# Kernel optimization log

Hardware: AMD Instinct MI355X
Metric: run time of the kernel (lower is better)

Reference implementation:

```python
import math
import jax, jax.numpy as jnp
import numpy as np

EMBED_DIM = 512
NUM_HEADS = 8
HEAD_DIM = EMBED_DIM // NUM_HEADS
NUM_EDGE_TYPES = 10
N = 2048  # nodes
B = 1


def setup_inputs() -> dict:
    key = jax.random.key(0)
    ks = jax.random.split(key, 8)
    s = 1.0 / math.sqrt(EMBED_DIM)
    return {
        "query": jax.random.normal(ks[0], (N, B, EMBED_DIM), jnp.float32),
        "key": jax.random.normal(ks[1], (N, B, EMBED_DIM), jnp.float32),
        "value": jax.random.normal(ks[2], (N, B, EMBED_DIM), jnp.float32),
        "edge_id_mat": jax.random.randint(ks[3], (N, N), 0, NUM_EDGE_TYPES, jnp.int32),
        "in_proj_weight": jax.random.normal(ks[4], (3 * EMBED_DIM, EMBED_DIM), jnp.float32) * s,
        "in_proj_bias": jnp.zeros((3 * EMBED_DIM,), jnp.float32),
        "out_proj_weight": jax.random.normal(ks[5], (EMBED_DIM, EMBED_DIM), jnp.float32) * s,
        "out_proj_bias": jnp.zeros((EMBED_DIM,), jnp.float32),
        "edge_embs_K": jax.random.normal(ks[6], (NUM_EDGE_TYPES, HEAD_DIM), jnp.float32),
    }


def reference(query, key, value, edge_id_mat, in_proj_weight, in_proj_bias,
              out_proj_weight, out_proj_bias, edge_embs_K):
    L, Bsz, E = query.shape
    H, hd = NUM_HEADS, HEAD_DIM
    w_q, w_k, w_v = jnp.split(in_proj_weight, 3, axis=0)
    b_q, b_k, b_v = jnp.split(in_proj_bias, 3)
    q = query @ w_q.T + b_q   # (L, B, E)
    k = key @ w_k.T + b_k
    v = value @ w_v.T + b_v

    def split_heads(x):
        # (L, B, E) -> (B*H, L, hd)  (matches torch view(L, B*H, hd).transpose(0,1))
        return x.reshape(L, Bsz * H, hd).transpose(1, 0, 2)

    q = split_heads(q) / math.sqrt(hd)  # torch scales by sqrt(E=head_dim)
    k = split_heads(k)
    v = split_heads(v)

    attn = jnp.einsum('bnd,bmd->bnm', q, k)  # (B*H, L, L)

    # edge-type score bias: edge_attn[b,i,j] = q[b,i,:] . edge_embs_K[edge_id_mat[i,j], :]
    # computed efficiently as per-type scores then a gather (avoids (L,L,hd) tensor)
    type_scores = jnp.einsum('bnd,td->bnt', q, edge_embs_K)  # (B*H, L, T)
    idx = jnp.broadcast_to(edge_id_mat[None, :, :], attn.shape)
    edge_attn = jnp.take_along_axis(type_scores, idx, axis=2)  # (B*H, L, L)
    attn = jax.nn.softmax(attn + edge_attn, axis=-1)

    out = jnp.einsum('bnm,bmd->bnd', attn, v)           # (B*H, L, hd)
    out = out.transpose(1, 0, 2).reshape(L, Bsz, E)      # (L, B, E)
    out = out @ out_proj_weight.T + out_proj_bias
    return out
```

## Files before the change

kernel.cpp:

```cpp
#include <hip/hip_runtime.h>
#include <hip/hip_bf16.h>

#define NHEAD 8
#define SEQ   2048
#define HD    64
#define EMB   512
#define NTYPE 10
#define JSPLIT 8

#define QKV_NT (3 * EMB / 64)
#define QKV_MT (SEQ / 64)
#define QKV_BLOCKS (QKV_NT * QKV_MT)
#define PACK_BLOCKS (SEQ * SEQ / 4 / 256)

#define QSCALE 0.180336878f

typedef unsigned short u16;
typedef __attribute__((ext_vector_type(8))) short short8;
typedef __attribute__((ext_vector_type(4))) short short4v;
typedef __attribute__((ext_vector_type(4))) float float4v;

union F8 { short8 v; uint4 u4; u16 us[8]; };
union PB { uint2 u2; short4v s4; };

__device__ __forceinline__ float bf2f(u16 u){
  union { unsigned u; float f; } w; w.u = ((unsigned)u) << 16; return w.f;
}
__device__ __forceinline__ u16 f2bf(float f){
  union { float f; unsigned u; } w; w.f = f;
  unsigned u = w.u;
  u += 0x7fffu + ((u >> 16) & 1u);
  return (u16)(u >> 16);
}
__device__ __forceinline__ unsigned cvtpk(float lo, float hi){
  union { __hip_bfloat162 b; unsigned u; } w;
  w.b = __float22bfloat162_rn(float2{lo, hi});
  return w.u;
}
__device__ __forceinline__ uint4 pk8(float4 a, float4 b){
  uint4 p; p.x = cvtpk(a.x, a.y); p.y = cvtpk(a.z, a.w);
           p.z = cvtpk(b.x, b.y); p.w = cvtpk(b.z, b.w);
  return p;
}

__device__ __forceinline__ void pv_mfma(float4v& ao, uint2 pa, uint2 vb){
#if __has_builtin(__builtin_amdgcn_mfma_f32_16x16x16bf16_1k)
  PB a; a.u2 = pa;
  PB b; b.u2 = vb;
  ao = __builtin_amdgcn_mfma_f32_16x16x16bf16_1k(a.s4, b.s4, ao, 0, 0, 0);
#else
  asm volatile("s_nop 1\n\tv_mfma_f32_16x16x16_bf16 %0, %1, %2, %0"
               : "+v"(ao) : "v"(pa), "v"(vb));
#endif
}

__global__ __launch_bounds__(256) void fused_prep_gemm(
    const float* __restrict__ q, const float* __restrict__ k, const float* __restrict__ v,
    const float* __restrict__ ipw, const float* __restrict__ ipb, const int* __restrict__ eid,
    u16* __restrict__ Qs, u16* __restrict__ Kb, u16* __restrict__ Vb,
    unsigned* __restrict__ eidp)
{
  const int b = blockIdx.x;
  const int t = threadIdx.x;

  if (b >= QKV_BLOCKS) {
    const int i = (b - QKV_BLOCKS) * 256 + t;
    int4 vv = ((const int4*)eid)[i];
    eidp[i] = (unsigned)(vv.x & 0xff) | ((unsigned)(vv.y & 0xff) << 8) |
              ((unsigned)(vv.z & 0xff) << 16) | ((unsigned)(vv.w & 0xff) << 24);
    return;
  }

  __shared__ u16 As[64][72];
  __shared__ u16 Bs[64][72];

  const int X = b & 7, jb = b >> 3;
  const int mt = X * 4 + (jb & 3), nt = jb >> 2;
  const int n0 = nt * 64, m0 = mt * 64;
  const int z = n0 >> 9;
  const float* A = (z == 0) ? q : (z == 1) ? k : v;
  const float scale = (z == 0) ? QSCALE : 1.0f;

  const int w = t >> 6, lane = t & 63, lr = lane & 15, lg = lane >> 4;
  const int wm = w >> 1, wn = w & 1;
  const int srow = t >> 2, kb16 = (t & 3) * 16;

  float4v acc[2][2];
#pragma unroll
  for (int mi = 0; mi < 2; mi++)
#pragma unroll
    for (int ni = 0; ni < 2; ni++) acc[mi][ni] = (float4v){0.f, 0.f, 0.f, 0.f};

  const float* pa = A   + (size_t)(m0 + srow) * EMB + kb16;
  const float* pw = ipw + (size_t)(n0 + srow) * EMB + kb16;

  float4 a[4], bb[4];
#pragma unroll
  for (int j = 0; j < 4; j++) { a[j] = *(const float4*)(pa + j * 4); bb[j] = *(const float4*)(pw + j * 4); }

  for (int k0 = 0; k0 < EMB; k0 += 64) {
    *(uint4*)&As[srow][kb16]     = pk8(a[0], a[1]);
    *(uint4*)&As[srow][kb16 + 8] = pk8(a[2], a[3]);
    *(uint4*)&Bs[srow][kb16]     = pk8(bb[0], bb[1]);
    *(uint4*)&Bs[srow][kb16 + 8] = pk8(bb[2], bb[3]);
    __syncthreads();
    if (k0 + 64 < EMB) {
#pragma unroll
      for (int j = 0; j < 4; j++) {
        a[j]  = *(const float4*)(pa + k0 + 64 + j * 4);
        bb[j] = *(const float4*)(pw + k0 + 64 + j * 4);
      }
    }
    F8 af[2][2], bf_[2][2];
#pragma unroll
    for (int kc = 0; kc < 2; kc++) {
#pragma unroll
      for (int mi = 0; mi < 2; mi++)
        af[mi][kc].u4 = *(const uint4*)&As[wm * 32 + mi * 16 + lr][kc * 32 + lg * 8];
#pragma unroll
      for (int ni = 0; ni < 2; ni++)
        bf_[ni][kc].u4 = *(const uint4*)&Bs[wn * 32 + ni * 16 + lr][kc * 32 + lg * 8];
    }
#pragma unroll
    for (int kc = 0; kc < 2; kc++)
#pragma unroll
      for (int mi = 0; mi < 2; mi++)
#pragma unroll
        for (int ni = 0; ni < 2; ni++)
          acc[mi][ni] = __builtin_amdgcn_mfma_f32_16x16x32_bf16(af[mi][kc].v, bf_[ni][kc].v, acc[mi][ni], 0, 0, 0);
    __syncthreads();
  }

  u16* O = (z == 0) ? Qs : ((z == 1) ? Kb : Vb);
#pragma unroll
  for (int mi = 0; mi < 2; mi++) {
#pragma unroll
    for (int ni = 0; ni < 2; ni++) {
      const int n = n0 + wn * 32 + ni * 16 + lr;
      const int e = n & 511, h = e >> 6, d = e & 63;
      const float bias = ipb[n];
      const int mb = m0 + wm * 32 + mi * 16 + lg * 4;
      if (z < 2) {
#pragma unroll
        for (int r = 0; r < 4; r++)
          O[((size_t)h * SEQ + mb + r) * HD + d] = f2bf((acc[mi][ni][r] + bias) * scale);
      } else {
        ushort4 pk;
        pk.x = f2bf(acc[mi][ni][0] + bias); pk.y = f2bf(acc[mi][ni][1] + bias);
        pk.z = f2bf(acc[mi][ni][2] + bias); pk.w = f2bf(acc[mi][ni][3] + bias);
        *(ushort4*)(O + ((size_t)(h * HD + d)) * SEQ + mb) = pk;
      }
    }
  }
}

__global__ __launch_bounds__(256) void attn_kernel(
    const u16* __restrict__ Qs, const u16* __restrict__ Kb, const u16* __restrict__ Vb,
    const unsigned* __restrict__ eid32, const float* __restrict__ EK,
    u16* __restrict__ Upart, float* __restrict__ mpart, float* __restrict__ lpart)
{
  __shared__ u16 Kt[64][72];
  __shared__ u16 Vt[64][72];
  __shared__ float tsl[64][13];
  __shared__ float ekl[NTYPE][64];

  const int t = threadIdx.x;
  const int wave = t >> 6, lane = t & 63, lr = lane & 15, lg = lane >> 4;
  const int bb_ = blockIdx.x;
  const int X = bb_ & 7, jj = bb_ >> 3;
  const int p = X * 8 + (jj >> 5);
  const int i0 = (jj & 31) * 64;
  const int h  = p >> 3;
  const int z  = p & 7;

  for (int i = t; i < NTYPE * 64; i += 256) ekl[i >> 6][i & 63] = EK[i];
  __syncthreads();

  {
    const int row = t >> 2, tt = t & 3;
    const u16* qr = Qs + ((size_t)h * SEQ + i0 + row) * HD;
    float a0 = 0.f, a1 = 0.f, a2 = 0.f;
    for (int d0 = 0; d0 < HD; d0 += 8) {
      uint4 qq = *(const uint4*)(qr + d0);
      const u16* qu = (const u16*)&qq;
#pragma unroll
      for (int e = 0; e < 8; e++) {
        float qf = bf2f(qu[e]);
        a0 += qf * ekl[tt][d0 + e];
        a1 += qf * ekl[tt + 4][d0 + e];
        a2 += qf * ekl[(tt < 2) ? (tt + 8) : 8][d0 + e];
      }
    }
    tsl[row][tt] = a0; tsl[row][tt + 4] = a1;
    if (tt < 2) tsl[row][tt + 8] = a2;
  }

  F8 qf[2];
#pragma unroll
  for (int kc = 0; kc < 2; kc++)
    qf[kc].u4 = *(const uint4*)(Qs + ((size_t)h * SEQ + i0 + wave * 16 + lr) * HD + kc * 32 + lg * 8);

  float4v ao[4];
#pragma unroll
  for (int d = 0; d < 4; d++) ao[d] = (float4v){0.f, 0.f, 0.f, 0.f};
  float m_i = -1e30f, l_i = 0.f;

  const int srow = t >> 2, sdc = (t & 3) * 16;
  const int jbase = z * (SEQ / JSPLIT);
  const int NT = (SEQ / JSPLIT) / 64;
  const unsigned* erow = eid32 + (size_t)(i0 + wave * 16 + lr) * (SEQ / 4);

  uint4 kp0, kp1, vp0, vp1;
  unsigned ed[4], edn[4];
  {
    const u16* kp = Kb + ((size_t)h * SEQ + jbase + srow) * HD + sdc;
    kp0 = *(const uint4*)kp; kp1 = *(const uint4*)(kp + 8);
    const u16* vp = Vb + ((size_t)(h * HD + srow)) * SEQ + jbase + sdc;
    vp0 = *(const uint4*)vp; vp1 = *(const uint4*)(vp + 8);
    *(uint4*)&Kt[srow][sdc] = kp0; *(uint4*)&Kt[srow][sdc + 8] = kp1;
    *(uint4*)&Vt[srow][sdc] = vp0; *(uint4*)&Vt[srow][sdc + 8] = vp1;
    const int ej = jbase >> 2;
#pragma unroll
    for (int c = 0; c < 4; c++) ed[c] = erow[ej + c * 4 + lg];
  }

  for (int jt = 0; jt < NT; jt++) {
    __syncthreads();

    if (jt + 1 < NT) {
      const int jn = jbase + (jt + 1) * 64;
      const u16* kp = Kb + ((size_t)h * SEQ + jn + srow) * HD + sdc;
      kp0 = *(const uint4*)kp; kp1 = *(const uint4*)(kp + 8);
      const u16* vp = Vb + ((size_t)(h * HD + srow)) * SEQ + jn + sdc;
      vp0 = *(const uint4*)vp; vp1 = *(const uint4*)(vp + 8);
      const int ejn = jn >> 2;
#pragma unroll
      for (int c = 0; c < 4; c++) edn[c] = erow[ejn + c * 4 + lg];
    }

    float4v sacc[4];
#pragma unroll
    for (int c = 0; c < 4; c++) sacc[c] = (float4v){0.f, 0.f, 0.f, 0.f};
#pragma unroll
    for (int kc = 0; kc < 2; kc++) {
#pragma unroll
      for (int c = 0; c < 4; c++) {
        F8 kf; kf.u4 = *(const uint4*)&Kt[c * 16 + lr][kc * 32 + lg * 8];
        sacc[c] = __builtin_amdgcn_mfma_f32_16x16x32_bf16(kf.v, qf[kc].v, sacc[c], 0, 0, 0);
      }
    }

    float rmax = -1e30f;
#pragma unroll
    for (int c = 0; c < 4; c++) {
      const unsigned e = ed[c];
#pragma unroll
      for (int r = 0; r < 4; r++) {
        const float s = sacc[c][r] + tsl[wave * 16 + lr][(e >> (r * 8)) & 0xffu];
        sacc[c][r] = s;
        rmax = fmaxf(rmax, s);
      }
    }
    rmax = fmaxf(rmax, __shfl_xor(rmax, 16));
    rmax = fmaxf(rmax, __shfl_xor(rmax, 32));
    const float mnew = fmaxf(m_i, rmax);
    const float fct = exp2f(m_i - mnew);
    float rsum = 0.f;
#pragma unroll
    for (int c = 0; c < 4; c++) {
#pragma unroll
      for (int r = 0; r < 4; r++) {
        const float p_ = exp2f(sacc[c][r] - mnew);
        sacc[c][r] = p_;
        rsum += p_;
      }
    }
    rsum += __shfl_xor(rsum, 16);
    rsum += __shfl_xor(rsum, 32);
    l_i = l_i * fct + rsum;
    m_i = mnew;

    uint2 pa_[4];
#pragma unroll
    for (int c = 0; c < 4; c++) {
      pa_[c].x = cvtpk(sacc[c][0], sacc[c][1]);
      pa_[c].y = cvtpk(sacc[c][2], sacc[c][3]);
    }
    float fctv[4];
#pragma unroll
    for (int rr = 0; rr < 4; rr++) fctv[rr] = __shfl(fct, lg * 4 + rr);
#pragma unroll
    for (int db = 0; db < 4; db++) {
#pragma unroll
      for (int rr = 0; rr < 4; rr++) ao[db][rr] *= fctv[rr];
    }
#pragma unroll
    for (int c = 0; c < 4; c++) {
#pragma unroll
      for (int db = 0; db < 4; db++) {
        uint2 vb = *(const uint2*)&Vt[db * 16 + lr][c * 16 + lg * 4];
        pv_mfma(ao[db], pa_[c], vb);
      }
    }

    __syncthreads();
    if (jt + 1 < NT) {
      *(uint4*)&Kt[srow][sdc] = kp0; *(uint4*)&Kt[srow][sdc + 8] = kp1;
      *(uint4*)&Vt[srow][sdc] = vp0; *(uint4*)&Vt[srow][sdc + 8] = vp1;
#pragma unroll
      for (int c = 0; c < 4; c++) ed[c] = edn[c];
    }
  }

  {
    const size_t base = (((size_t)z * NHEAD + h) * SEQ + i0) * HD;
#pragma unroll
    for (int db = 0; db < 4; db++) {
#pragma unroll
      for (int rr = 0; rr < 4; rr++) {
        const int n = wave * 16 + lg * 4 + rr;
        Upart[base + (size_t)n * HD + db * 16 + lr] = f2bf(ao[db][rr]);
      }
    }
    if (lg == 0) {
      mpart[((size_t)z * NHEAD + h) * SEQ + i0 + wave * 16 + lr] = m_i;
      lpart[((size_t)z * NHEAD + h) * SEQ + i0 + wave * 16 + lr] = l_i;
    }
  }
}

__global__ __launch_bounds__(256) void combine_outproj(
    const u16* __restrict__ Upart, const float* __restrict__ mpart,
    const float* __restrict__ lpart, const float* __restrict__ opw,
    const float* __restrict__ opb, float* __restrict__ out)
{
  __shared__ u16 As[32][72];
  __shared__ u16 Bs[64][72];
  __shared__ float cww[JSPLIT][NHEAD][32];

  const int t = threadIdx.x;
  const int b = blockIdx.x;
  const int X = b & 7, jb = b >> 3;
  const int mt = X * 8 + (jb >> 3), nt = jb & 7;
  const int m0 = mt * 32, n0 = nt * 64;

  {
    const int hh = t >> 5, nl = t & 31;
    const int gn = m0 + nl;
    float mz[JSPLIT], wz[JSPLIT];
    float M = -1e30f;
#pragma unroll
    for (int zz = 0; zz < JSPLIT; zz++) {
      mz[zz] = mpart[((size_t)zz * NHEAD + hh) * SEQ + gn];
      M = fmaxf(M, mz[zz]);
    }
    float Ls = 0.f;
#pragma unroll
    for (int zz = 0; zz < JSPLIT; zz++) {
      wz[zz] = exp2f(mz[zz] - M);
      Ls += wz[zz] * lpart[((size_t)zz * NHEAD + hh) * SEQ + gn];
    }
    const float inv = 1.0f / Ls;
#pragma unroll
    for (int zz = 0; zz < JSPLIT; zz++) cww[zz][hh][nl] = wz[zz] * inv;
  }
  __syncthreads();

  const int w = t >> 6, lane = t & 63, lr = lane & 15, lg = lane >> 4;
  const int arow = t >> 3, akb = (t & 7) * 8;
  const int brow = t >> 2, bkb = (t & 3) * 16;

  float4v acc[2];
#pragma unroll
  for (int mi = 0; mi < 2; mi++) acc[mi] = (float4v){0.f, 0.f, 0.f, 0.f};

  const float* pw = opw + (size_t)(n0 + brow) * EMB + bkb;

  int hcur = akb >> 6, dcur = akb & 63;
  uint4 ua[JSPLIT];
#pragma unroll
  for (int zz = 0; zz < JSPLIT; zz++)
    ua[zz] = *(const uint4*)(Upart + (((size_t)zz * NHEAD + hcur) * SEQ + m0 + arow) * HD + dcur);
  float4 bbv[4];
#pragma unroll
  for (int j = 0; j < 4; j++) bbv[j] = *(const float4*)(pw + j * 4);

  for (int k0 = 0; k0 < EMB; k0 += 64) {
    {
      float cc[8];
#pragma unroll
      for (int j = 0; j < 8; j++) cc[j] = 0.f;
#pragma unroll
      for (int zz = 0; zz < JSPLIT; zz++) {
        const float wgt = cww[zz][hcur][arow];
        F8 q0; q0.u4 = ua[zz];
#pragma unroll
        for (int j = 0; j < 8; j++) cc[j] += wgt * bf2f((u16)q0.us[j]);
      }
      float4 c0 = {cc[0], cc[1], cc[2], cc[3]}, c1 = {cc[4], cc[5], cc[6], cc[7]};
      *(uint4*)&As[arow][akb] = pk8(c0, c1);
      *(uint4*)&Bs[brow][bkb]     = pk8(bbv[0], bbv[1]);
      *(uint4*)&Bs[brow][bkb + 8] = pk8(bbv[2], bbv[3]);
    }
    __syncthreads();
    if (k0 + 64 < EMB) {
      const int e = k0 + 64 + akb;
      hcur = e >> 6; dcur = e & 63;
#pragma unroll
      for (int zz = 0; zz < JSPLIT; zz++)
        ua[zz] = *(const uint4*)(Upart + (((size_t)zz * NHEAD + hcur) * SEQ + m0 + arow) * HD + dcur);
#pragma unroll
      for (int j = 0; j < 4; j++) bbv[j] = *(const float4*)(pw + k0 + 64 + j * 4);
    }
    F8 af[2][2], bf_[2];
#pragma unroll
    for (int kc = 0; kc < 2; kc++) {
#pragma unroll
      for (int mi = 0; mi < 2; mi++)
        af[mi][kc].u4 = *(const uint4*)&As[mi * 16 + lr][kc * 32 + lg * 8];
      bf_[kc].u4 = *(const uint4*)&Bs[w * 16 + lr][kc * 32 + lg * 8];
    }
#pragma unroll
    for (int kc = 0; kc < 2; kc++)
#pragma unroll
      for (int mi = 0; mi < 2; mi++)
        acc[mi] = __builtin_amdgcn_mfma_f32_16x16x32_bf16(af[mi][kc].v, bf_[kc].v, acc[mi], 0, 0, 0);
    __syncthreads();
  }

  const int n = n0 + w * 16 + lr;
  const float bias = opb[n];
#pragma unroll
  for (int mi = 0; mi < 2; mi++) {
    const int mb = m0 + mi * 16 + lg * 4;
#pragma unroll
    for (int r = 0; r < 4; r++)
      out[(size_t)(mb + r) * EMB + n] = acc[mi][r] + bias;
  }
}

extern "C" void kernel_launch(void* const* d_in, const int* in_sizes, int n_in,
                              void* d_out, int out_size, void* d_ws, size_t ws_size,
                              hipStream_t stream)
{
  const float* query = (const float*)d_in[0];
  const float* key_  = (const float*)d_in[1];
  const float* value = (const float*)d_in[2];
  const int*   eid   = (const int*)d_in[3];
  const float* ipw   = (const float*)d_in[4];
  const float* ipb   = (const float*)d_in[5];
  const float* opw   = (const float*)d_in[6];
  const float* opb   = (const float*)d_in[7];
  const float* ek    = (const float*)d_in[8];
  float* out = (float*)d_out;

  char* ws = (char*)d_ws;
  u16* Qs = (u16*)ws;              ws += (size_t)NHEAD * SEQ * HD * 2;
  u16* Kb = (u16*)ws;              ws += (size_t)NHEAD * SEQ * HD * 2;
  u16* Vb = (u16*)ws;              ws += (size_t)NHEAD * SEQ * HD * 2;
  unsigned* eidp = (unsigned*)ws;  ws += (size_t)SEQ * SEQ;
  u16* Upart = (u16*)ws;           ws += (size_t)JSPLIT * NHEAD * SEQ * HD * 2;
  float* mpart = (float*)ws;       ws += (size_t)JSPLIT * NHEAD * SEQ * 4;
  float* lpart = (float*)ws;       ws += (size_t)JSPLIT * NHEAD * SEQ * 4;

  fused_prep_gemm<<<dim3(QKV_BLOCKS + PACK_BLOCKS), dim3(256), 0, stream>>>(
      query, key_, value, ipw, ipb, eid, Qs, Kb, Vb, eidp);
  attn_kernel<<<dim3(SEQ / 64 * NHEAD * JSPLIT), dim3(256), 0, stream>>>(
      Qs, Kb, Vb, eidp, ek, Upart, mpart, lpart);
  combine_outproj<<<dim3((SEQ / 32) * (EMB / 64)), dim3(256), 0, stream>>>(
      Upart, mpart, lpart, opw, opb, out);
}
```

Before: 153.5 us.

## Drop LDS staging in attention, use MFMA for edge scores, halve J-split

```diff
diff --git a/kernel.cpp b/kernel.cpp
--- a/kernel.cpp
+++ b/kernel.cpp
@@ -6,12 +6,14 @@
 #define HD    64
 #define EMB   512
 #define NTYPE 10
-#define JSPLIT 8
+#define JSPLIT 4
 
 #define QKV_NT (3 * EMB / 64)
 #define QKV_MT (SEQ / 64)
 #define QKV_BLOCKS (QKV_NT * QKV_MT)
 #define PACK_BLOCKS (SEQ * SEQ / 4 / 256)
+#define OPW_BLOCKS (EMB * EMB / 8 / 256)
+#define PREP_BLOCKS (QKV_BLOCKS + PACK_BLOCKS + OPW_BLOCKS + 1)
 
 #define QSCALE 0.180336878f
 
@@ -57,17 +59,35 @@
 __global__ __launch_bounds__(256) void fused_prep_gemm(
     const float* __restrict__ q, const float* __restrict__ k, const float* __restrict__ v,
     const float* __restrict__ ipw, const float* __restrict__ ipb, const int* __restrict__ eid,
+    const float* __restrict__ opw, const float* __restrict__ ek,
     u16* __restrict__ Qs, u16* __restrict__ Kb, u16* __restrict__ Vb,
-    unsigned* __restrict__ eidp)
+    unsigned* __restrict__ eidp, u16* __restrict__ opwb, u16* __restrict__ EKb)
 {
   const int b = blockIdx.x;
   const int t = threadIdx.x;
 
   if (b >= QKV_BLOCKS) {
-    const int i = (b - QKV_BLOCKS) * 256 + t;
-    int4 vv = ((const int4*)eid)[i];
-    eidp[i] = (unsigned)(vv.x & 0xff) | ((unsigned)(vv.y & 0xff) << 8) |
-              ((unsigned)(vv.z & 0xff) << 16) | ((unsigned)(vv.w & 0xff) << 24);
+    if (b < QKV_BLOCKS + PACK_BLOCKS) {
+      const int i = (b - QKV_BLOCKS) * 256 + t;
+      int4 vv = ((const int4*)eid)[i];
+      eidp[i] = (unsigned)(vv.x & 0xff) | ((unsigned)(vv.y & 0xff) << 8) |
+                ((unsigned)(vv.z & 0xff) << 16) | ((unsigned)(vv.w & 0xff) << 24);
+    } else if (b < QKV_BLOCKS + PACK_BLOCKS + OPW_BLOCKS) {
+      const int i = (b - QKV_BLOCKS - PACK_BLOCKS) * 256 + t;
+      float4 a = *(const float4*)(opw + i * 8);
+      float4 c = *(const float4*)(opw + i * 8 + 4);
+      *(uint4*)(opwb + i * 8) = pk8(a, c);
+    } else {
+      const int gi = t * 4;
+      ushort4 pk;
+      u16* pp = (u16*)&pk;
+#pragma unroll
+      for (int e = 0; e < 4; e++) {
+        const int type = (gi + e) >> 6, d = (gi + e) & 63;
+        pp[e] = f2bf(type < NTYPE ? ek[type * HD + d] : 0.f);
+      }
+      *(ushort4*)(EKb + gi) = pk;
+    }
     return;
   }
 
@@ -156,99 +176,69 @@
 
 __global__ __launch_bounds__(256) void attn_kernel(
     const u16* __restrict__ Qs, const u16* __restrict__ Kb, const u16* __restrict__ Vb,
-    const unsigned* __restrict__ eid32, const float* __restrict__ EK,
+    const unsigned* __restrict__ eid32, const u16* __restrict__ EKb,
     u16* __restrict__ Upart, float* __restrict__ mpart, float* __restrict__ lpart)
 {
-  __shared__ u16 Kt[64][72];
-  __shared__ u16 Vt[64][72];
-  __shared__ float tsl[64][13];
-  __shared__ float ekl[NTYPE][64];
+  __shared__ float tsl[4][16][18];
 
   const int t = threadIdx.x;
   const int wave = t >> 6, lane = t & 63, lr = lane & 15, lg = lane >> 4;
   const int bb_ = blockIdx.x;
   const int X = bb_ & 7, jj = bb_ >> 3;
-  const int p = X * 8 + (jj >> 5);
+  const int p = X * 4 + (jj >> 5);
   const int i0 = (jj & 31) * 64;
-  const int h  = p >> 3;
-  const int z  = p & 7;
-
-  for (int i = t; i < NTYPE * 64; i += 256) ekl[i >> 6][i & 63] = EK[i];
-  __syncthreads();
+  const int h  = p >> 2;
+  const int z  = p & 3;
+
+  const int irow = i0 + wave * 16 + lr;
+
+  F8 qf[2];
+#pragma unroll
+  for (int kc = 0; kc < 2; kc++)
+    qf[kc].u4 = *(const uint4*)(Qs + ((size_t)h * SEQ + irow) * HD + kc * 32 + lg * 8);
 
   {
-    const int row = t >> 2, tt = t & 3;
-    const u16* qr = Qs + ((size_t)h * SEQ + i0 + row) * HD;
-    float a0 = 0.f, a1 = 0.f, a2 = 0.f;
-    for (int d0 = 0; d0 < HD; d0 += 8) {
-      uint4 qq = *(const uint4*)(qr + d0);
-      const u16* qu = (const u16*)&qq;
-#pragma unroll
-      for (int e = 0; e < 8; e++) {
-        float qf = bf2f(qu[e]);
-        a0 += qf * ekl[tt][d0 + e];
-        a1 += qf * ekl[tt + 4][d0 + e];
-        a2 += qf * ekl[(tt < 2) ? (tt + 8) : 8][d0 + e];
-      }
-    }
-    tsl[row][tt] = a0; tsl[row][tt + 4] = a1;
-    if (tt < 2) tsl[row][tt + 8] = a2;
-  }
-
-  F8 qf[2];
-#pragma unroll
-  for (int kc = 0; kc < 2; kc++)
-    qf[kc].u4 = *(const uint4*)(Qs + ((size_t)h * SEQ + i0 + wave * 16 + lr) * HD + kc * 32 + lg * 8);
+    float4v ts = (float4v){0.f, 0.f, 0.f, 0.f};
+#pragma unroll
+    for (int kc = 0; kc < 2; kc++) {
+      F8 ekf; ekf.u4 = *(const uint4*)(EKb + lr * HD + kc * 32 + lg * 8);
+      ts = __builtin_amdgcn_mfma_f32_16x16x32_bf16(ekf.v, qf[kc].v, ts, 0, 0, 0);
+    }
+    *(float2*)&tsl[wave][lr][lg * 4]     = float2{ts[0], ts[1]};
+    *(float2*)&tsl[wave][lr][lg * 4 + 2] = float2{ts[2], ts[3]};
+  }
 
   float4v ao[4];
 #pragma unroll
   for (int d = 0; d < 4; d++) ao[d] = (float4v){0.f, 0.f, 0.f, 0.f};
   float m_i = -1e30f, l_i = 0.f;
 
-  const int srow = t >> 2, sdc = (t & 3) * 16;
+  const u16* kbase = Kb + (size_t)h * SEQ * HD;
+  const u16* vbase = Vb + (size_t)h * HD * SEQ;
+  const unsigned* erow = eid32 + (size_t)irow * (SEQ / 4);
   const int jbase = z * (SEQ / JSPLIT);
-  const int NT = (SEQ / JSPLIT) / 64;
-  const unsigned* erow = eid32 + (size_t)(i0 + wave * 16 + lr) * (SEQ / 4);
-
-  uint4 kp0, kp1, vp0, vp1;
-  unsigned ed[4], edn[4];
-  {
-    const u16* kp = Kb + ((size_t)h * SEQ + jbase + srow) * HD + sdc;
-    kp0 = *(const uint4*)kp; kp1 = *(const uint4*)(kp + 8);
-    const u16* vp = Vb + ((size_t)(h * HD + srow)) * SEQ + jbase + sdc;
-    vp0 = *(const uint4*)vp; vp1 = *(const uint4*)(vp + 8);
-    *(uint4*)&Kt[srow][sdc] = kp0; *(uint4*)&Kt[srow][sdc + 8] = kp1;
-    *(uint4*)&Vt[srow][sdc] = vp0; *(uint4*)&Vt[srow][sdc + 8] = vp1;
-    const int ej = jbase >> 2;
-#pragma unroll
-    for (int c = 0; c < 4; c++) ed[c] = erow[ej + c * 4 + lg];
-  }
-
-  for (int jt = 0; jt < NT; jt++) {
-    __syncthreads();
-
-    if (jt + 1 < NT) {
-      const int jn = jbase + (jt + 1) * 64;
-      const u16* kp = Kb + ((size_t)h * SEQ + jn + srow) * HD + sdc;
-      kp0 = *(const uint4*)kp; kp1 = *(const uint4*)(kp + 8);
-      const u16* vp = Vb + ((size_t)(h * HD + srow)) * SEQ + jn + sdc;
-      vp0 = *(const uint4*)vp; vp1 = *(const uint4*)(vp + 8);
-      const int ejn = jn >> 2;
-#pragma unroll
-      for (int c = 0; c < 4; c++) edn[c] = erow[ejn + c * 4 + lg];
+
+  for (int jt = 0; jt < (SEQ / JSPLIT) / 64; jt++) {
+    const int j0 = jbase + jt * 64;
+
+    F8 kf[4][2];
+    unsigned ed[4];
+#pragma unroll
+    for (int c = 0; c < 4; c++) {
+#pragma unroll
+      for (int kc = 0; kc < 2; kc++)
+        kf[c][kc].u4 = *(const uint4*)(kbase + (size_t)(j0 + c * 16 + lr) * HD + kc * 32 + lg * 8);
+      ed[c] = erow[(j0 >> 2) + c * 4 + lg];
     }
 
     float4v sacc[4];
 #pragma unroll
     for (int c = 0; c < 4; c++) sacc[c] = (float4v){0.f, 0.f, 0.f, 0.f};
 #pragma unroll
-    for (int kc = 0; kc < 2; kc++) {
-#pragma unroll
-      for (int c = 0; c < 4; c++) {
-        F8 kf; kf.u4 = *(const uint4*)&Kt[c * 16 + lr][kc * 32 + lg * 8];
-        sacc[c] = __builtin_amdgcn_mfma_f32_16x16x32_bf16(kf.v, qf[kc].v, sacc[c], 0, 0, 0);
-      }
-    }
+    for (int kc = 0; kc < 2; kc++)
+#pragma unroll
+      for (int c = 0; c < 4; c++)
+        sacc[c] = __builtin_amdgcn_mfma_f32_16x16x32_bf16(kf[c][kc].v, qf[kc].v, sacc[c], 0, 0, 0);
 
     float rmax = -1e30f;
 #pragma unroll
@@ -256,7 +246,7 @@
       const unsigned e = ed[c];
 #pragma unroll
       for (int r = 0; r < 4; r++) {
-        const float s = sacc[c][r] + tsl[wave * 16 + lr][(e >> (r * 8)) & 0xffu];
+        const float s = sacc[c][r] + tsl[wave][lr][(e >> (r * 8)) & 0xffu];
         sacc[c][r] = s;
         rmax = fmaxf(rmax, s);
       }
@@ -290,25 +280,17 @@
 #pragma unroll
     for (int rr = 0; rr < 4; rr++) fctv[rr] = __shfl(fct, lg * 4 + rr);
 #pragma unroll
-    for (int db = 0; db < 4; db++) {
+    for (int db = 0; db < 4; db++)
 #pragma unroll
       for (int rr = 0; rr < 4; rr++) ao[db][rr] *= fctv[rr];
-    }
+
 #pragma unroll
     for (int c = 0; c < 4; c++) {
 #pragma unroll
       for (int db = 0; db < 4; db++) {
-        uint2 vb = *(const uint2*)&Vt[db * 16 + lr][c * 16 + lg * 4];
+        uint2 vb = *(const uint2*)(vbase + (size_t)(db * 16 + lr) * SEQ + j0 + c * 16 + lg * 4);
         pv_mfma(ao[db], pa_[c], vb);
       }
-    }
-
-    __syncthreads();
-    if (jt + 1 < NT) {
-      *(uint4*)&Kt[srow][sdc] = kp0; *(uint4*)&Kt[srow][sdc + 8] = kp1;
-      *(uint4*)&Vt[srow][sdc] = vp0; *(uint4*)&Vt[srow][sdc + 8] = vp1;
-#pragma unroll
-      for (int c = 0; c < 4; c++) ed[c] = edn[c];
     }
   }
 
@@ -323,15 +305,15 @@
       }
     }
     if (lg == 0) {
-      mpart[((size_t)z * NHEAD + h) * SEQ + i0 + wave * 16 + lr] = m_i;
-      lpart[((size_t)z * NHEAD + h) * SEQ + i0 + wave * 16 + lr] = l_i;
+      mpart[((size_t)z * NHEAD + h) * SEQ + irow] = m_i;
+      lpart[((size_t)z * NHEAD + h) * SEQ + irow] = l_i;
     }
   }
 }
 
 __global__ __launch_bounds__(256) void combine_outproj(
     const u16* __restrict__ Upart, const float* __restrict__ mpart,
-    const float* __restrict__ lpart, const float* __restrict__ opw,
+    const float* __restrict__ lpart, const u16* __restrict__ opwb,
     const float* __restrict__ opb, float* __restrict__ out)
 {
   __shared__ u16 As[32][72];
@@ -374,16 +356,14 @@
 #pragma unroll
   for (int mi = 0; mi < 2; mi++) acc[mi] = (float4v){0.f, 0.f, 0.f, 0.f};
 
-  const float* pw = opw + (size_t)(n0 + brow) * EMB + bkb;
+  const u16* pw = opwb + (size_t)(n0 + brow) * EMB + bkb;
 
   int hcur = akb >> 6, dcur = akb & 63;
   uint4 ua[JSPLIT];
 #pragma unroll
   for (int zz = 0; zz < JSPLIT; zz++)
     ua[zz] = *(const uint4*)(Upart + (((size_t)zz * NHEAD + hcur) * SEQ + m0 + arow) * HD + dcur);
-  float4 bbv[4];
-#pragma unroll
-  for (int j = 0; j < 4; j++) bbv[j] = *(const float4*)(pw + j * 4);
+  uint4 bb0 = *(const uint4*)pw, bb1 = *(const uint4*)(pw + 8);
 
   for (int k0 = 0; k0 < EMB; k0 += 64) {
     {
@@ -399,8 +379,8 @@
       }
       float4 c0 = {cc[0], cc[1], cc[2], cc[3]}, c1 = {cc[4], cc[5], cc[6], cc[7]};
       *(uint4*)&As[arow][akb] = pk8(c0, c1);
-      *(uint4*)&Bs[brow][bkb]     = pk8(bbv[0], bbv[1]);
-      *(uint4*)&Bs[brow][bkb + 8] = pk8(bbv[2], bbv[3]);
+      *(uint4*)&Bs[brow][bkb]     = bb0;
+      *(uint4*)&Bs[brow][bkb + 8] = bb1;
     }
     __syncthreads();
     if (k0 + 64 < EMB) {
@@ -409,8 +389,8 @@
 #pragma unroll
       for (int zz = 0; zz < JSPLIT; zz++)
         ua[zz] = *(const uint4*)(Upart + (((size_t)zz * NHEAD + hcur) * SEQ + m0 + arow) * HD + dcur);
-#pragma unroll
-      for (int j = 0; j < 4; j++) bbv[j] = *(const float4*)(pw + k0 + 64 + j * 4);
+      bb0 = *(const uint4*)(pw + k0 + 64);
+      bb1 = *(const uint4*)(pw + k0 + 64 + 8);
     }
     F8 af[2][2], bf_[2];
 #pragma unroll
@@ -462,11 +442,13 @@
   u16* Upart = (u16*)ws;           ws += (size_t)JSPLIT * NHEAD * SEQ * HD * 2;
   float* mpart = (float*)ws;       ws += (size_t)JSPLIT * NHEAD * SEQ * 4;
   float* lpart = (float*)ws;       ws += (size_t)JSPLIT * NHEAD * SEQ * 4;
-
-  fused_prep_gemm<<<dim3(QKV_BLOCKS + PACK_BLOCKS), dim3(256), 0, stream>>>(
-      query, key_, value, ipw, ipb, eid, Qs, Kb, Vb, eidp);
+  u16* opwb = (u16*)ws;            ws += (size_t)EMB * EMB * 2;
+  u16* EKb  = (u16*)ws;            ws += (size_t)16 * HD * 2;
+
+  fused_prep_gemm<<<dim3(PREP_BLOCKS), dim3(256), 0, stream>>>(
+      query, key_, value, ipw, ipb, eid, opw, ek, Qs, Kb, Vb, eidp, opwb, EKb);
   attn_kernel<<<dim3(SEQ / 64 * NHEAD * JSPLIT), dim3(256), 0, stream>>>(
-      Qs, Kb, Vb, eidp, ek, Upart, mpart, lpart);
+      Qs, Kb, Vb, eidp, EKb, Upart, mpart, lpart);
   combine_outproj<<<dim3((SEQ / 32) * (EMB / 64)), dim3(256), 0, stream>>>(
-      Upart, mpart, lpart, opw, opb, out);
-}
+      Upart, mpart, lpart, opwb, opb, out);
+}
```

New measurement: 210.4 us. 1.37x slower.
